# Optimization experiments

Measured on AMD Instinct MI355X. Metric: run time of the kernel, lower is better.

Reference implementation:

```python
import jax, jax.numpy as jnp
import numpy as np
from jax import lax

C = 64; H = 128; W = 256; HW = H * W
HIDDEN = 64
D_STATE = 64; HEADDIM = 64; EXPAND = 2; CHUNK = 256; CONV_K = 4
D_INNER = EXPAND * C            # 128
NHEADS = D_INNER // HEADDIM     # 2
CONV_DIM = D_INNER + 2 * D_STATE  # 256
D_IN_PROJ = 2 * D_INNER + 2 * D_STATE + NHEADS  # 386
RECORD_LEN = [5, 3, 4, 2]
EPS = 1e-5


def setup_inputs() -> dict:
    key = jax.random.key(0)
    ks = jax.random.split(key, 16)
    def nrm(k, shape, scale=0.02):
        return scale * jax.random.normal(k, shape, jnp.float32)
    return {
        "xx": jax.random.normal(ks[0], (sum(RECORD_LEN), C, H, W), jnp.float32),
        "record_len": jnp.array(RECORD_LEN, jnp.int32),
        "score_w1": nrm(ks[1], (HIDDEN, C)),
        "score_b1": jnp.zeros((HIDDEN,), jnp.float32),
        "score_w2": nrm(ks[2], (1, HIDDEN)),
        "score_b2": jnp.zeros((1,), jnp.float32),
        "q_w": nrm(ks[3], (C, C)), "q_b": jnp.zeros((C,), jnp.float32),
        "k_w": nrm(ks[4], (C, C)), "k_b": jnp.zeros((C,), jnp.float32),
        "v_w": nrm(ks[5], (C, C)), "v_b": jnp.zeros((C,), jnp.float32),
        "ln_w": jnp.ones((C,), jnp.float32), "ln_b": jnp.zeros((C,), jnp.float32),
        "in_proj_w": nrm(ks[6], (D_IN_PROJ, C)),
        "in_proj_b": jnp.zeros((D_IN_PROJ,), jnp.float32),
        "conv_w": nrm(ks[7], (CONV_DIM, 1, CONV_K), 0.1),
        "conv_b": jnp.zeros((CONV_DIM,), jnp.float32),
        "dt_bias": 0.1 * jax.random.normal(ks[8], (NHEADS,), jnp.float32),
        "A_log": jnp.log(jnp.arange(1, NHEADS + 1, dtype=jnp.float32)),
        "ssd_D": jnp.ones((NHEADS,), jnp.float32),
        "rms_w": jnp.ones((D_INNER,), jnp.float32),
        "out_proj_w": nrm(ks[9], (C, D_INNER)),
    }


def _segsum(x):
    # x: (..., T) -> (..., T, T) with sum_{j<k<=i} x[k] below diagonal, -inf above
    T = x.shape[-1]
    cs = jnp.cumsum(x, -1)
    ss = cs[..., :, None] - cs[..., None, :]
    return jnp.where(jnp.tril(jnp.ones((T, T), bool)), ss, -jnp.inf)


def _ssd(x, A, Bm, Cm):
    # Mamba2 chunked SSD. x:(b,l,h,p) pre-scaled by dt; A:(b,l,h)=dt*A_head; Bm,Cm:(b,l,n) (ngroups=1)
    b, l, h, p = x.shape
    c = l // CHUNK
    x = x.reshape(b, c, CHUNK, h, p)
    A = A.reshape(b, c, CHUNK, h).transpose(0, 3, 1, 2)            # (b,h,c,cl)
    Bm = Bm.reshape(b, c, CHUNK, -1)
    Cm = Cm.reshape(b, c, CHUNK, -1)
    A_cum = jnp.cumsum(A, -1)
    Lmat = jnp.exp(_segsum(A))                                     # (b,h,c,cl,cl)
    Y_diag = jnp.einsum('bcln,bcsn,bhcls,bcshp->bclhp', Cm, Bm, Lmat, x)
    decay_states = jnp.exp(A_cum[..., -1:] - A_cum)                # (b,h,c,cl)
    states = jnp.einsum('bcln,bhcl,bclhp->bchpn', Bm, decay_states, x)
    padded = jnp.pad(A_cum[..., -1], ((0, 0), (0, 0), (1, 0)))     # (b,h,c+1)
    decay_chunk = jnp.exp(_segsum(padded))                         # (b,h,c+1,c+1)
    states_cat = jnp.concatenate([jnp.zeros_like(states[:, :1]), states], 1)
    states_in = jnp.einsum('bhzc,bchpn->bzhpn', decay_chunk, states_cat)[:, :-1]
    Y_off = jnp.einsum('bcln,bchpn,bhcl->bclhp', Cm, states_in, jnp.exp(A_cum))
    return (Y_diag + Y_off).reshape(b, l, h, p)


def _forward(xx, record_len, score_w1, score_b1, score_w2, score_b2,
             q_w, q_b, k_w, k_b, v_w, v_b, ln_w, ln_b,
             in_proj_w, in_proj_b, conv_w, conv_b,
             dt_bias, A_log, ssd_D, rms_w, out_proj_w):
    rl = [int(v) for v in np.asarray(record_len)]
    # score_mlp: 1x1 convs == per-pixel channel MLP, applied to all CAVs at once
    s = jax.nn.relu(jnp.einsum('nchw,dc->ndhw', xx, score_w1) + score_b1[None, :, None, None])
    scores = (jnp.einsum('ndhw,od->nohw', s, score_w2) + score_b2[None, :, None, None])[:, 0]  # (N,H,W)
    fused = []
    start = 0
    for n in rl:  # ragged groups (variable n_cav per sample)
        grp_sc = scores[start:start + n]
        idx = jnp.argmax(grp_sc, axis=0)  # topk k=1; softmax over singleton -> weight 1
        fused.append(jnp.take_along_axis(xx[start:start + n], idx[None, None], axis=0)[0])
        start += n
    fused = jnp.stack(fused)  # (B,C,H,W)
    Bsz = fused.shape[0]
    seq = fused.reshape(Bsz, C, HW).transpose(0, 2, 1)  # (B,L,C)
    # ScaledDotProductAttention on (HW,1,C): each position attends only to itself
    q = seq @ q_w.T + q_b
    k = seq @ k_w.T + k_b
    v = seq @ v_w.T + v_b
    score = jnp.sum(q * k, -1, keepdims=True) / np.float32(np.sqrt(C))  # (B,L,1)
    attn = jax.nn.softmax(score[..., None], axis=-1)[..., 0]            # == 1
    ctx = attn * v
    # VMAMBA2 block: pre-LayerNorm -> Mamba2 SSD -> residual
    mu = jnp.mean(ctx, -1, keepdims=True)
    var = jnp.var(ctx, -1, keepdims=True)
    u = (ctx - mu) / jnp.sqrt(var + EPS) * ln_w + ln_b
    zxbcdt = u @ in_proj_w.T + in_proj_b
    z = zxbcdt[..., :D_INNER]
    xBC = zxbcdt[..., D_INNER:D_INNER + CONV_DIM]
    dt = zxbcdt[..., D_INNER + CONV_DIM:]
    xBC = lax.conv_general_dilated(xBC.transpose(0, 2, 1), conv_w, (1,), [(CONV_K - 1, 0)],
                                   dimension_numbers=('NCH', 'OIH', 'NCH'),
                                   feature_group_count=CONV_DIM)
    xBC = jax.nn.silu(xBC + conv_b[None, :, None]).transpose(0, 2, 1)  # (B,L,CONV_DIM)
    xh = xBC[..., :D_INNER].reshape(Bsz, HW, NHEADS, HEADDIM)
    Bm = xBC[..., D_INNER:D_INNER + D_STATE]
    Cm = xBC[..., D_INNER + D_STATE:]
    dt = jax.nn.softplus(dt + dt_bias)  # (B,L,h)
    A = -jnp.exp(A_log)                 # (h,)
    y = _ssd(xh * dt[..., None], dt * A, Bm, Cm)
    y = y + ssd_D[None, None, :, None] * xh
    y = y.reshape(Bsz, HW, D_INNER)
    yz = y * jax.nn.silu(z)             # gated RMSNorm
    y = yz * lax.rsqrt(jnp.mean(yz * yz, -1, keepdims=True) + EPS) * rms_w
    h = ctx + y @ out_proj_w.T
    return h.transpose(0, 2, 1).reshape(Bsz, C, H, W)


def reference(xx, record_len, score_w1, score_b1, score_w2, score_b2,
              q_w, q_b, k_w, k_b, v_w, v_b, ln_w, ln_b,
              in_proj_w, in_proj_b, conv_w, conv_b,
              dt_bias, A_log, ssd_D, rms_w, out_proj_w):
    return _forward(xx, record_len, score_w1, score_b1, score_w2, score_b2,
                    q_w, q_b, k_w, k_b, v_w, v_b, ln_w, ln_b,
                    in_proj_w, in_proj_b, conv_w, conv_b,
                    dt_bias, A_log, ssd_D, rms_w, out_proj_w)
```

## Files before the change

### kernel.cpp

```cpp
#include <hip/hip_runtime.h>
#include <cmath>

#define HW 32768
#define NC 128
#define NH 2
#define B4 4

typedef __attribute__((ext_vector_type(8))) short bf16x8;
typedef __attribute__((ext_vector_type(4))) float f32x4;
typedef __attribute__((ext_vector_type(4))) ushort u16x4;
typedef __attribute__((ext_vector_type(8))) ushort u16x8;

__device__ __forceinline__ ushort f2b(float x) {
  union { float f; unsigned u; } v; v.f = x;
  unsigned r = v.u + 0x7FFFu + ((v.u >> 16) & 1u);
  return (ushort)(r >> 16);
}
__device__ __forceinline__ float b2f(ushort b) {
  union { unsigned u; float f; } v; v.u = ((unsigned)b) << 16;
  return v.f;
}
__device__ __forceinline__ int swz(int row, int k) { return k ^ ((row & 7) << 3); }
__device__ __forceinline__ bf16x8 ldfrag(const ushort* base, int row, int k, int stride) {
  return *(const bf16x8*)(base + row * stride + swz(row, k));
}

__global__ __launch_bounds__(256) void k_score_mfma(
    const float* __restrict__ xx, const float* __restrict__ w1,
    const float* __restrict__ b1, const float* __restrict__ w2,
    const float* __restrict__ b2, float* __restrict__ scores,
    int* __restrict__ cnt)
{
  __shared__ ushort Whi[64*64];
  __shared__ ushort Wlo[64*64];
  __shared__ ushort Xt[4][64*64];
  __shared__ float w2b1[128];
  int tid = threadIdx.x;
  if (blockIdx.x == 0 && tid == 0) cnt[0] = 0;
  for (int i = tid; i < 4096; i += 256) {
    int d = i >> 6, c = i & 63;
    float v = w1[i];
    ushort hi = f2b(v);
    int off = d*64 + swz(d, c);
    Whi[off] = hi;
    Wlo[off] = f2b(v - b2f(hi));
  }
  if (tid < 64) { w2b1[tid] = w2[tid]; w2b1[64+tid] = b1[tid]; }

  int wid = tid >> 6, lane = tid & 63;
  int n  = blockIdx.x >> 7;
  int t0 = (blockIdx.x & 127)*256 + wid*64;

  {
    const float* px = xx + (size_t)n*64*HW + t0 + lane;
    float xv[64];
    #pragma unroll
    for (int c = 0; c < 64; ++c) xv[c] = px[(size_t)c*HW];
    ushort* xh = Xt[wid];
    #pragma unroll
    for (int c8 = 0; c8 < 8; ++c8) {
      u16x8 p;
      #pragma unroll
      for (int j = 0; j < 8; ++j) p[j] = f2b(xv[c8*8 + j]);
      *(u16x8*)(xh + lane*64 + swz(lane, c8*8)) = p;
    }
  }
  __syncthreads();

  int lr = lane & 15, kb = lane >> 4;
  const ushort* xh = Xt[wid];
  f32x4 acc[4][4];
  #pragma unroll
  for (int m = 0; m < 4; ++m)
    #pragma unroll
    for (int nt = 0; nt < 4; ++nt) acc[m][nt] = (f32x4){0.f,0.f,0.f,0.f};
  #pragma unroll
  for (int k0 = 0; k0 < 64; k0 += 32) {
    bf16x8 ah[4], al[4], bx[4];
    #pragma unroll
    for (int m = 0; m < 4; ++m) {
      ah[m] = ldfrag(Whi, 16*m + lr, k0 + kb*8, 64);
      al[m] = ldfrag(Wlo, 16*m + lr, k0 + kb*8, 64);
    }
    #pragma unroll
    for (int nt = 0; nt < 4; ++nt) bx[nt] = ldfrag(xh, 16*nt + lr, k0 + kb*8, 64);
    #pragma unroll
    for (int m = 0; m < 4; ++m)
      #pragma unroll
      for (int nt = 0; nt < 4; ++nt) {
        acc[m][nt] = __builtin_amdgcn_mfma_f32_16x16x32_bf16(ah[m], bx[nt], acc[m][nt], 0, 0, 0);
        acc[m][nt] = __builtin_amdgcn_mfma_f32_16x16x32_bf16(al[m], bx[nt], acc[m][nt], 0, 0, 0);
      }
  }
  float bb2 = b2[0];
  #pragma unroll
  for (int nt = 0; nt < 4; ++nt) {
    float s = 0.f;
    #pragma unroll
    for (int m = 0; m < 4; ++m)
      #pragma unroll
      for (int r = 0; r < 4; ++r) {
        int d = 16*m + kb*4 + r;
        float h = acc[m][nt][r] + w2b1[64 + d];
        s += fmaxf(h, 0.f) * w2b1[d];
      }
    s += __shfl_xor(s, 16);
    s += __shfl_xor(s, 32);
    if (kb == 0) scores[(size_t)n*HW + t0 + 16*nt + lr] = s + bb2;
  }
}

__global__ __launch_bounds__(256) void k_argmax(
    const float* __restrict__ scores, int* __restrict__ idx,
    int* __restrict__ cnt, int* __restrict__ list)
{
  int i = blockIdx.x*256 + threadIdx.x;
  int g = i >> 15, t = i & (HW-1);
  const int gs0[4] = {0,5,8,12};
  const int gl0[4] = {5,3,4,2};
  int start = gs0[g], len = gl0[g];
  float best = scores[(size_t)start*HW + t];
  float second = -3.4e38f;
  int bi = start;
  for (int j = 1; j < len; ++j) {
    float s = scores[(size_t)(start+j)*HW + t];
    if (s > best) { second = best; best = s; bi = start + j; }
    else if (s > second) second = s;
  }
  idx[i] = bi;
  if (best - second < 5e-4f) {
    int p = atomicAdd(cnt, 1);
    list[p] = i;
  }
}

__global__ __launch_bounds__(256) void k_fix(
    const float* __restrict__ xx, const float* __restrict__ w1,
    const float* __restrict__ b1, const float* __restrict__ w2,
    const float* __restrict__ b2, const int* __restrict__ cnt,
    const int* __restrict__ list, int* __restrict__ idx)
{
  __shared__ float w1f[64*65];
  __shared__ float w2f[64], b1f[64];
  int tid = threadIdx.x;
  for (int i = tid; i < 4096; i += 256) w1f[(i >> 6)*65 + (i & 63)] = w1[i];
  if (tid < 64) { w2f[tid] = w2[tid]; b1f[tid] = b1[tid]; }
  __syncthreads();
  int n = cnt[0];
  int wid = tid >> 6, lane = tid & 63;
  int nwaves = gridDim.x * 4;
  const int gs0[4] = {0,5,8,12};
  const int gl0[4] = {5,3,4,2};
  double b2d = (double)b2[0];
  for (int e = blockIdx.x*4 + wid; e < n; e += nwaves) {
    int i = list[e];
    int g = i >> 15, t = i & (HW-1);
    int start = gs0[g], len = gl0[g];
    double best = -1e300;
    int bi = start;
    for (int j = 0; j < len; ++j) {
      double xv = (double)xx[(size_t)(start+j)*64*HW + (size_t)lane*HW + t];
      double acc = (double)b1f[lane];
      #pragma unroll
      for (int c = 0; c < 64; ++c) {
        double xc = __shfl(xv, c);
        acc += xc * (double)w1f[lane*65 + c];
      }
      double sc = (acc > 0.0 ? acc : 0.0) * (double)w2f[lane];
      #pragma unroll
      for (int m = 1; m < 64; m <<= 1) sc += __shfl_xor(sc, m);
      sc += b2d;
      if (sc > best) { best = sc; bi = start + j; }
    }
    if (lane == 0) idx[i] = bi;
  }
}

__global__ __launch_bounds__(256) void k_fuse(
    const float* __restrict__ xx, const int* __restrict__ idx,
    float* __restrict__ seq)
{
  __shared__ int idxs[64];
  __shared__ float tile[64*65];
  int tid = threadIdx.x;
  int g  = blockIdx.x >> 9;
  int t0 = (blockIdx.x & 511) << 6;
  if (tid < 64) idxs[tid] = idx[(size_t)g*HW + t0 + tid];
  __syncthreads();
  int tl = tid & 63, cq = tid >> 6;
  for (int r = 0; r < 16; ++r) {
    int c = r*4 + cq;
    tile[c*65 + tl] = xx[(size_t)idxs[tl]*64*HW + (size_t)c*HW + t0 + tl];
  }
  __syncthreads();
  for (int r = 0; r < 16; ++r) {
    int row = r*4 + cq;
    seq[((size_t)g*HW + t0 + row)*64 + tl] = tile[tl*65 + row];
  }
}

__global__ __launch_bounds__(256) void k_vln(
    const float* __restrict__ seq, const float* __restrict__ vw,
    const float* __restrict__ vb, const float* __restrict__ lnw,
    const float* __restrict__ lnb, float* __restrict__ ctx,
    ushort* __restrict__ usw)
{
  __shared__ float st[64*64];
  int tid = threadIdx.x;
  size_t p0 = (size_t)blockIdx.x * 64;
  for (int i = tid; i < 64*64; i += 256) st[i] = seq[p0*64 + i];
  int o = tid & 63, wv = tid >> 6;
  float w[64];
  const float4* w4 = (const float4*)(vw + o*64);
  #pragma unroll
  for (int c4 = 0; c4 < 16; ++c4) {
    float4 v = w4[c4];
    w[c4*4+0]=v.x; w[c4*4+1]=v.y; w[c4*4+2]=v.z; w[c4*4+3]=v.w;
  }
  float bias = vb[o], lw = lnw[o], lb = lnb[o];
  __syncthreads();
  const float4* st4 = (const float4*)st;
  for (int j = 0; j < 16; ++j) {
    int p = wv*16 + j;
    float acc = bias;
    #pragma unroll
    for (int c4 = 0; c4 < 16; ++c4) {
      float4 s4 = st4[p*16 + c4];
      acc += s4.x*w[c4*4] + s4.y*w[c4*4+1] + s4.z*w[c4*4+2] + s4.w*w[c4*4+3];
    }
    float s1 = acc, s2 = acc*acc;
    #pragma unroll
    for (int m = 1; m < 64; m <<= 1) {
      s1 += __shfl_xor(s1, m);
      s2 += __shfl_xor(s2, m);
    }
    float mu  = s1*(1.f/64.f);
    float var = s2*(1.f/64.f) - mu*mu;
    float rstd = rsqrtf(var + 1e-5f);
    size_t base = (p0+p)*64;
    int gt = (int)(p0 + p);
    ctx[base + o] = acc;
    usw[base + (o ^ (((gt+3)&7)<<3))] = f2b((acc - mu)*rstd*lw + lb);
  }
}

__global__ __launch_bounds__(256) void k_prep(
    const float* __restrict__ ipw, ushort* __restrict__ wsw)
{
  int i = blockIdx.x*256 + threadIdx.x;
  int row = i >> 6, c = i & 63;
  float v = (row < 386) ? ipw[row*64 + c] : 0.f;
  wsw[row*64 + swz(row, c)] = f2b(v);
}

__global__ __launch_bounds__(512) void k_gemm(
    const ushort* __restrict__ usw, const ushort* __restrict__ wsw,
    const float* __restrict__ ipb, const float* __restrict__ dtbias,
    ushort* __restrict__ z, ushort* __restrict__ xbcB, float* __restrict__ dt)
{
  __shared__ ushort Wlds[400*64];
  __shared__ ushort Ulds[80*64];
  __shared__ ushort trans[8704];
  int tid = threadIdx.x;
  int b     = blockIdx.x >> 7;
  int chunk = blockIdx.x & 127;
  int w = tid >> 6, lane = tid & 63, lr = lane & 15, kb = lane >> 4;

  for (int i = tid; i < 3200; i += 512)
    *(u16x8*)(Wlds + i*8) = *(const u16x8*)(wsw + i*8);

  for (int it = 0; it < 4; ++it) {
    int s = chunk*4 + it;
    int t0 = s << 6;
    size_t pixbase = (size_t)b*HW + t0;
    size_t tilebase = ((size_t)(b*512 + s))*256*64;
    {
      const ushort* ubase = usw + ((size_t)b*HW + t0 - 3)*64;
      for (int i = tid; i < 536; i += 512) {
        u16x8 v;
        if (t0 == 0 && i < 24) v = (u16x8){0,0,0,0,0,0,0,0};
        else v = *(const u16x8*)(ubase + i*8);
        *(u16x8*)(Ulds + i*8) = v;
      }
    }
    __syncthreads();

    for (int rd = 0; rd < 3; ++rd) {
      int nt = rd*8 + w;
      f32x4 acc[5];
      #pragma unroll
      for (int mt = 0; mt < 5; ++mt) acc[mt] = (f32x4){0.f,0.f,0.f,0.f};
      #pragma unroll
      for (int kk = 0; kk < 64; kk += 32) {
        bf16x8 bfrag = ldfrag(Wlds, nt*16 + lr, kk + kb*8, 64);
        #pragma unroll
        for (int mt = 0; mt < 5; ++mt) {
          bf16x8 afrag = ldfrag(Ulds, mt*16 + lr, kk + kb*8, 64);
          acc[mt] = __builtin_amdgcn_mfma_f32_16x16x32_bf16(afrag, bfrag, acc[mt], 0, 0, 0);
        }
      }
      float bias = ipb[nt*16 + lr];
      if (rd == 0) {
        #pragma unroll
        for (int mt = 0; mt < 5; ++mt)
          #pragma unroll
          for (int r = 0; r < 4; ++r) {
            int t = mt*16 + kb*4 + r - 3;
            if (t >= 0 && t < 64) trans[t*132 + w*16 + lr] = f2b(acc[mt][r] + bias);
          }
      } else {
        #pragma unroll
        for (int mt = 0; mt < 5; ++mt)
          #pragma unroll
          for (int r = 0; r < 4; ++r) {
            int t = mt*16 + kb*4 + r - 3;
            if (t >= 0 && t < 64) trans[(w*16 + lr)*68 + t] = f2b(acc[mt][r] + bias);
          }
      }
      __syncthreads();
      if (rd == 0) {
        for (int i = tid; i < 2048; i += 512) {
          int t = i >> 5, c4 = (i & 31)*4;
          *(u16x4*)(z + (pixbase + t)*128 + c4) = *(const u16x4*)(trans + t*132 + c4);
        }
      } else {
        int chbase = (rd - 1)*128;
        for (int i = tid; i < 2048; i += 512) {
          int ch = i >> 4, t4 = (i & 15)*4;
          *(u16x4*)(xbcB + tilebase + (size_t)(chbase + ch)*64 + t4)
              = *(const u16x4*)(trans + ch*68 + t4);
        }
      }
      __syncthreads();
    }

    if (w == 0) {
      f32x4 acc[5];
      #pragma unroll
      for (int mt = 0; mt < 5; ++mt) acc[mt] = (f32x4){0.f,0.f,0.f,0.f};
      #pragma unroll
      for (int kk = 0; kk < 64; kk += 32) {
        bf16x8 bfrag = ldfrag(Wlds, 384 + lr, kk + kb*8, 64);
        #pragma unroll
        for (int mt = 0; mt < 5; ++mt) {
          bf16x8 afrag = ldfrag(Ulds, mt*16 + lr, kk + kb*8, 64);
          acc[mt] = __builtin_amdgcn_mfma_f32_16x16x32_bf16(afrag, bfrag, acc[mt], 0, 0, 0);
        }
      }
      if (lr < 2) {
        float bias = ipb[384 + lr] + dtbias[lr];
        #pragma unroll
        for (int mt = 0; mt < 5; ++mt)
          #pragma unroll
          for (int r = 0; r < 4; ++r) {
            int t = mt*16 + kb*4 + r - 3;
            if (t >= 0 && t < 64) {
              float a = acc[mt][r] + bias;
              dt[(pixbase + t)*2 + lr] = (a > 20.f) ? a : log1pf(expf(a));
            }
          }
      }
    }
    __syncthreads();
  }
}

__global__ __launch_bounds__(256) void k_conv(
    const ushort* __restrict__ xbcB, const float* __restrict__ convw,
    const float* __restrict__ convb, ushort* __restrict__ co2,
    ushort* __restrict__ Bm, ushort* __restrict__ Cm)
{
  __shared__ ushort bmc[64*132];
  int tid = threadIdx.x;
  int b  = blockIdx.x >> 9;
  int s  = blockIdx.x & 511;
  int lane = tid & 63, wv = tid >> 6;
  int toct = lane & 7, chi = lane >> 3;
  size_t tilebase = ((size_t)(b*512 + s))*256*64;
  const ushort* tsrc = xbcB + tilebase;
  const ushort* psrc = xbcB + tilebase - 256*64;

  for (int it = 0; it < 8; ++it) {
    int ch = wv*64 + it*8 + chi;
    u16x8 v = *(const u16x8*)(tsrc + ch*64 + toct*8);
    float x0 = b2f(v[0]), x1 = b2f(v[1]), x2 = b2f(v[2]), x3 = b2f(v[3]);
    float x4 = b2f(v[4]), x5 = b2f(v[5]), x6 = b2f(v[6]), x7 = b2f(v[7]);
    float pm1 = __shfl(x7, lane - 1);
    float pm2 = __shfl(x6, lane - 1);
    float pm3 = __shfl(x5, lane - 1);
    if (toct == 0) {
      if (s > 0) {
        u16x4 hq = *(const u16x4*)(psrc + ch*64 + 60);
        pm3 = b2f(hq[1]); pm2 = b2f(hq[2]); pm1 = b2f(hq[3]);
      } else {
        pm1 = pm2 = pm3 = 0.f;
      }
    }
    float4 cw = ((const float4*)convw)[ch];
    float cb = convb[ch];
    float o0 = cb + cw.x*pm3 + cw.y*pm2 + cw.z*pm1 + cw.w*x0;
    float o1 = cb + cw.x*pm2 + cw.y*pm1 + cw.z*x0  + cw.w*x1;
    float o2 = cb + cw.x*pm1 + cw.y*x0  + cw.z*x1  + cw.w*x2;
    float o3 = cb + cw.x*x0  + cw.y*x1  + cw.z*x2  + cw.w*x3;
    float o4 = cb + cw.x*x1  + cw.y*x2  + cw.z*x3  + cw.w*x4;
    float o5 = cb + cw.x*x2  + cw.y*x3  + cw.z*x4  + cw.w*x5;
    float o6 = cb + cw.x*x3  + cw.y*x4  + cw.z*x5  + cw.w*x6;
    float o7 = cb + cw.x*x4  + cw.y*x5  + cw.z*x6  + cw.w*x7;
    u16x8 ov;
    ov[0] = f2b(o0 / (1.f + __expf(-o0)));
    ov[1] = f2b(o1 / (1.f + __expf(-o1)));
    ov[2] = f2b(o2 / (1.f + __expf(-o2)));
    ov[3] = f2b(o3 / (1.f + __expf(-o3)));
    ov[4] = f2b(o4 / (1.f + __expf(-o4)));
    ov[5] = f2b(o5 / (1.f + __expf(-o5)));
    ov[6] = f2b(o6 / (1.f + __expf(-o6)));
    ov[7] = f2b(o7 / (1.f + __expf(-o7)));
    *(u16x8*)(co2 + tilebase + (size_t)ch*64 + toct*8) = ov;
    if (ch >= 128) {
      int c = ch - 128;
      int csw = c ^ (toct << 2);
      #pragma unroll
      for (int j = 0; j < 8; ++j)
        bmc[(toct*8 + j)*132 + csw] = ov[j];
    }
  }
  __syncthreads();
  size_t tg = (size_t)b*HW + s*64;
  for (int i = tid; i < 1024; i += 256) {
    int tt = i >> 4, n4 = (i & 15)*4;
    int sw = (tt >> 3) << 2;
    *(u16x4*)(Bm + (tg + tt)*64 + n4) = *(const u16x4*)(bmc + tt*132 + (n4 ^ sw));
    *(u16x4*)(Cm + (tg + tt)*64 + n4) = *(const u16x4*)(bmc + tt*132 + ((64 + n4) ^ sw));
  }
}

__global__ __launch_bounds__(256) void k_states(
    const float* __restrict__ dt, const ushort* __restrict__ co2,
    const float* __restrict__ A_log,
    float* __restrict__ states, float* __restrict__ A_last)
{
  extern __shared__ char smem[];
  float* ac  = (float*)smem;
  float* dec = ac + 256;
  ushort* xdT = (ushort*)(dec + 256);
  ushort* BT  = xdT + 16384;
  int tid = threadIdx.x;
  int ci = blockIdx.x, h = blockIdx.y, b = blockIdx.z;
  size_t tg = (size_t)b*HW + (size_t)ci*256;
  float Aneg = -expf(A_log[h]);
  float dv = dt[(tg + tid)*2 + h];
  ac[tid] = dv*Aneg;
  __syncthreads();
  for (int off = 1; off < 256; off <<= 1) {
    float v = (tid >= off) ? ac[tid - off] : 0.f;
    __syncthreads();
    ac[tid] += v;
    __syncthreads();
  }
  float alast = ac[255];
  dec[tid] = dv * __expf(alast - ac[tid]);
  __syncthreads();
  for (int i = tid; i < 64*32; i += 256) {
    int p = i >> 5, lc = (i & 31) * 8;
    int s = (ci << 2) + (lc >> 6);
    const ushort* cb2 = co2 + ((size_t)(b*512 + s))*256*64 + (lc & 63);
    u16x8 xv = *(const u16x8*)(cb2 + (size_t)(h*64 + p)*64);
    u16x8 o;
    #pragma unroll
    for (int e = 0; e < 8; ++e) o[e] = f2b(b2f(xv[e]) * dec[lc + e]);
    *(u16x8*)(xdT + p*256 + swz(p, lc)) = o;
    u16x8 bv = *(const u16x8*)(cb2 + (size_t)(128 + p)*64);
    *(u16x8*)(BT + p*256 + swz(p, lc)) = bv;
  }
  __syncthreads();
  int w = tid >> 6, lane = tid & 63, lr = lane & 15, kb = lane >> 4;
  f32x4 acc[4];
  #pragma unroll
  for (int m = 0; m < 4; ++m) acc[m] = (f32x4){0.f,0.f,0.f,0.f};
  for (int k0 = 0; k0 < 256; k0 += 32) {
    bf16x8 bfrag = ldfrag(BT, 16*w + lr, k0 + kb*8, 256);
    #pragma unroll
    for (int m = 0; m < 4; ++m) {
      bf16x8 afrag = ldfrag(xdT, 16*m + lr, k0 + kb*8, 256);
      acc[m] = __builtin_amdgcn_mfma_f32_16x16x32_bf16(afrag, bfrag, acc[m], 0, 0, 0);
    }
  }
  size_t sb = (((size_t)b*NC + ci)*NH + h)*4096;
  #pragma unroll
  for (int m = 0; m < 4; ++m)
    #pragma unroll
    for (int r = 0; r < 4; ++r)
      states[sb + (size_t)(16*m + kb*4 + r)*64 + 16*w + lr] = acc[m][r];
  if (tid == 0) A_last[((size_t)b*NH + h)*NC + ci] = alast;
}

__global__ __launch_bounds__(256) void k_scan(
    const float* __restrict__ states, const float* __restrict__ A_last,
    float* __restrict__ states_in)
{
  __shared__ float ef[NC];
  int tid = threadIdx.x;
  int seg = blockIdx.x & 7, h = (blockIdx.x >> 3) & 1, b = blockIdx.x >> 4;
  if (tid < NC) ef[tid] = __expf(A_last[((size_t)b*NH + h)*NC + tid]);
  __syncthreads();
  size_t base0 = (((size_t)b*NC)*NH + h)*4096 + seg*512 + tid;
  const size_t cstride = (size_t)NH*4096;
  float s0 = 0.f, s1 = 0.f;
  float ld0 = states[base0], ld1 = states[base0 + 256];
  for (int zc = 0; zc < NC; ++zc) {
    size_t cur = base0 + (size_t)zc*cstride;
    float n0 = 0.f, n1 = 0.f;
    if (zc < NC-1) { n0 = states[cur + cstride]; n1 = states[cur + cstride + 256]; }
    states_in[cur] = s0; states_in[cur + 256] = s1;
    float e = ef[zc];
    s0 = ld0 + e*s0; s1 = ld1 + e*s1;
    ld0 = n0; ld1 = n1;
  }
}

__global__ __launch_bounds__(512) void k_ydiag(
    const float* __restrict__ dt, const ushort* __restrict__ co2,
    const ushort* __restrict__ Bm, const ushort* __restrict__ Cm,
    const float* __restrict__ states_in, const float* __restrict__ A_log,
    const float* __restrict__ ssd_D, ushort* __restrict__ y)
{
  extern __shared__ char smem[];
  float* ac   = (float*)smem;
  float* dts  = ac + 256;
  float* segs = dts + 256;
  ushort* Cb  = (ushort*)(segs + 8);
  ushort* Bb  = Cb + 16384;
  ushort* xsT = Bb + 16384;
  ushort* Sb  = xsT + 16384;
  ushort* Wb  = Sb + 4096;
  int tid = threadIdx.x;
  int ci = blockIdx.x, h = blockIdx.y, b = blockIdx.z;
  size_t tg = (size_t)b*HW + (size_t)ci*256;
  int w = tid >> 6, lane = tid & 63, lr = lane & 15, kb = lane >> 4;
  float Aneg = -expf(A_log[h]);

  float dv = 0.f, a = 0.f;
  if (tid < 256) {
    dv = dt[(tg + tid)*2 + h];
    a = dv*Aneg;
    #pragma unroll
    for (int d = 1; d < 64; d <<= 1) {
      float t = __shfl_up(a, d);
      if (lane >= d) a += t;
    }
    if (lane == 63) segs[w] = a;
  }
  __syncthreads();
  if (tid < 256) {
    float off = 0.f;
    #pragma unroll
    for (int j = 0; j < 4; ++j) if (j < w) off += segs[j];
    ac[tid] = a + off;
    dts[tid] = dv;
  }

  for (int i = tid; i < 256*16; i += 512) {
    int l = i >> 4, n4 = (i & 15) * 4;
    u16x4 cv = *(const u16x4*)(Cm + (tg + l)*64 + n4);
    *(u16x4*)(Cb + l*64 + swz(l, n4)) = cv;
    u16x4 bv = *(const u16x4*)(Bm + (tg + l)*64 + n4);
    *(u16x4*)(Bb + l*64 + swz(l, n4)) = bv;
  }
  {
    const ushort* ct0 = co2 + ((size_t)(b*512 + (ci << 2)))*16384 + (size_t)h*4096;
    for (int i = tid; i < 64*32; i += 512) {
      int p = i >> 5, sc = (i & 31) * 8;
      u16x8 xv = *(const u16x8*)(ct0 + (size_t)(sc >> 6)*16384 + (size_t)p*64 + (sc & 63));
      *(u16x8*)(xsT + p*256 + swz(p, sc)) = xv;
    }
  }
  size_t sbg = (((size_t)b*NC + ci)*NH + h)*4096;
  for (int i = tid; i < 1024; i += 512) {
    int p = i >> 4, n4 = (i & 15) * 4;
    float4 sv = *(const float4*)(states_in + sbg + p*64 + n4);
    u16x4 pk = { f2b(sv.x), f2b(sv.y), f2b(sv.z), f2b(sv.w) };
    *(u16x4*)(Sb + p*64 + swz(p, n4)) = pk;
  }
  __syncthreads();

  int strips[2] = { w, 15 - w };
  ushort* Ww = Wb + w*1152;

  f32x4 yy[2][4];
  #pragma unroll
  for (int sp = 0; sp < 2; ++sp)
    #pragma unroll
    for (int n = 0; n < 4; ++n) yy[sp][n] = (f32x4){0.f,0.f,0.f,0.f};
  #pragma unroll
  for (int kk = 0; kk < 64; kk += 32) {
    bf16x8 af[2], bf[4];
    #pragma unroll
    for (int sp = 0; sp < 2; ++sp) af[sp] = ldfrag(Cb, strips[sp]*16 + lr, kk + kb*8, 64);
    #pragma unroll
    for (int n = 0; n < 4; ++n) bf[n] = ldfrag(Sb, 16*n + lr, kk + kb*8, 64);
    #pragma unroll
    for (int sp = 0; sp < 2; ++sp)
      #pragma unroll
      for (int n = 0; n < 4; ++n)
        yy[sp][n] = __builtin_amdgcn_mfma_f32_16x16x32_bf16(af[sp], bf[n], yy[sp][n], 0, 0, 0);
  }
  #pragma unroll
  for (int sp = 0; sp < 2; ++sp)
    #pragma unroll
    for (int r = 0; r < 4; ++r) {
      float e = __expf(ac[strips[sp]*16 + kb*4 + r]);
      #pragma unroll
      for (int n = 0; n < 4; ++n) yy[sp][n][r] *= e;
    }

  #pragma unroll
  for (int sp = 0; sp < 2; ++sp) {
    int strip = strips[sp];
    int l0 = strip*16;
    int nst = (strip >> 2) + 1;
    for (int st = 0; st < nst; ++st) {
      int s0 = st*64;
      f32x4 g[4];
      #pragma unroll
      for (int n = 0; n < 4; ++n) g[n] = (f32x4){0.f,0.f,0.f,0.f};
      #pragma unroll
      for (int kk = 0; kk < 64; kk += 32) {
        bf16x8 af = ldfrag(Cb, l0 + lr, kk + kb*8, 64);
        bf16x8 bf[4];
        #pragma unroll
        for (int n = 0; n < 4; ++n) bf[n] = ldfrag(Bb, s0 + 16*n + lr, kk + kb*8, 64);
        #pragma unroll
        for (int n = 0; n < 4; ++n)
          g[n] = __builtin_amdgcn_mfma_f32_16x16x32_bf16(af, bf[n], g[n], 0, 0, 0);
      }
      #pragma unroll
      for (int r = 0; r < 4; ++r) {
        int lrow = kb*4 + r;
        int lg = l0 + lrow;
        float acl = ac[lg];
        #pragma unroll
        for (int n = 0; n < 4; ++n) {
          int sl = 16*n + lr;
          int sg = s0 + sl;
          float v = (sg <= lg) ? g[n][r] * __expf(acl - ac[sg]) * dts[sg] : 0.f;
          Ww[lrow*72 + sl] = f2b(v);
        }
      }
      #pragma unroll
      for (int kk = 0; kk < 64; kk += 32) {
        bf16x8 af = *(const bf16x8*)(Ww + lr*72 + kk + kb*8);
        bf16x8 bf[4];
        #pragma unroll
        for (int n = 0; n < 4; ++n) bf[n] = ldfrag(xsT, 16*n + lr, s0 + kk + kb*8, 256);
        #pragma unroll
        for (int n = 0; n < 4; ++n)
          yy[sp][n] = __builtin_amdgcn_mfma_f32_16x16x32_bf16(af, bf[n], yy[sp][n], 0, 0, 0);
      }
    }
  }

  float Dh = ssd_D[h];
  #pragma unroll
  for (int sp = 0; sp < 2; ++sp)
    #pragma unroll
    for (int r = 0; r < 4; ++r) {
      int lg = strips[sp]*16 + kb*4 + r;
      #pragma unroll
      for (int n = 0; n < 4; ++n) {
        int p = 16*n + lr;
        float val = yy[sp][n][r] + Dh * b2f(xsT[p*256 + swz(p, lg)]);
        y[(tg + lg)*128 + h*64 + p] = f2b(val);
      }
    }
}

__global__ __launch_bounds__(256) void k_final(
    const ushort* __restrict__ y, const ushort* __restrict__ z,
    const float* __restrict__ ctx, const float* __restrict__ rms_w,
    const float* __restrict__ opw, float* __restrict__ out)
{
  __shared__ ushort yn[64*128];
  __shared__ ushort wop[64*128];
  __shared__ float otile[64*65];
  int tid = threadIdx.x;
  size_t p0 = (size_t)blockIdx.x * 64;

  for (int i = tid; i < 2048; i += 256) {
    int row = i >> 5, c4 = (i & 31) * 4;
    float4 v = ((const float4*)(opw + row*128))[c4 >> 2];
    float4 rw = ((const float4*)rms_w)[c4 >> 2];
    u16x4 p = { f2b(v.x*rw.x), f2b(v.y*rw.y), f2b(v.z*rw.z), f2b(v.w*rw.w) };
    *(u16x4*)(wop + row*128 + swz(row, c4)) = p;
  }

  {
    int t = tid >> 2, q = tid & 3;
    const u16x4* yp = (const u16x4*)(y + (p0 + t)*128 + q*32);
    const u16x4* zp = (const u16x4*)(z + (p0 + t)*128 + q*32);
    float vals[32];
    float ss = 0.f;
    #pragma unroll
    for (int j = 0; j < 8; ++j) {
      u16x4 yv = yp[j];
      u16x4 zv = zp[j];
      #pragma unroll
      for (int e = 0; e < 4; ++e) {
        float zf = b2f(zv[e]);
        float x = b2f(yv[e]) * (zf / (1.f + __expf(-zf)));
        vals[j*4+e] = x; ss += x*x;
      }
    }
    ss += __shfl_xor(ss, 1);
    ss += __shfl_xor(ss, 2);
    float rinv = rsqrtf(ss*(1.f/128.f) + 1e-5f);
    #pragma unroll
    for (int j = 0; j < 8; ++j) {
      int c4 = q*32 + j*4;
      u16x4 p = { f2b(vals[j*4]*rinv), f2b(vals[j*4+1]*rinv),
                  f2b(vals[j*4+2]*rinv), f2b(vals[j*4+3]*rinv) };
      *(u16x4*)(yn + t*128 + swz(t, c4)) = p;
    }
  }
  __syncthreads();

  int w = tid >> 6, lane = tid & 63, lr = lane & 15, kb = lane >> 4;
  f32x4 acc[4];
  #pragma unroll
  for (int n = 0; n < 4; ++n) acc[n] = (f32x4){0.f,0.f,0.f,0.f};
  #pragma unroll
  for (int kk = 0; kk < 128; kk += 32) {
    bf16x8 a = ldfrag(yn, w*16 + lr, kk + kb*8, 128);
    #pragma unroll
    for (int n = 0; n < 4; ++n) {
      bf16x8 bf = ldfrag(wop, n*16 + lr, kk + kb*8, 128);
      acc[n] = __builtin_amdgcn_mfma_f32_16x16x32_bf16(a, bf, acc[n], 0, 0, 0);
    }
  }
  #pragma unroll
  for (int n = 0; n < 4; ++n)
    #pragma unroll
    for (int r = 0; r < 4; ++r) {
      int tok = w*16 + kb*4 + r, ch = n*16 + lr;
      otile[ch*65 + tok] = acc[n][r] + ctx[(p0 + tok)*64 + ch];
    }
  __syncthreads();
  {
    size_t b  = p0 >> 15;
    size_t t0 = p0 & (HW-1);
    for (int r = 0; r < 16; ++r) {
      int cc = r*4 + (tid >> 6);
      int pp = tid & 63;
      out[(b*64 + cc)*HW + t0 + pp] = otile[cc*65 + pp];
    }
  }
}

extern "C" void kernel_launch(void* const* d_in, const int* in_sizes, int n_in,
                              void* d_out, int out_size, void* d_ws, size_t ws_size,
                              hipStream_t stream) {
  (void)in_sizes; (void)n_in; (void)out_size; (void)ws_size;
  const float* xx   = (const float*)d_in[0];
  const float* sw1  = (const float*)d_in[2];
  const float* sb1  = (const float*)d_in[3];
  const float* sw2  = (const float*)d_in[4];
  const float* sb2  = (const float*)d_in[5];
  const float* vw   = (const float*)d_in[10];
  const float* vb   = (const float*)d_in[11];
  const float* lnw  = (const float*)d_in[12];
  const float* lnb  = (const float*)d_in[13];
  const float* ipw  = (const float*)d_in[14];
  const float* ipb  = (const float*)d_in[15];
  const float* cw   = (const float*)d_in[16];
  const float* cb   = (const float*)d_in[17];
  const float* dtb  = (const float*)d_in[18];
  const float* alog = (const float*)d_in[19];
  const float* sd   = (const float*)d_in[20];
  const float* rmsw = (const float*)d_in[21];
  const float* opw  = (const float*)d_in[22];

  float* ws = (float*)d_ws;
  float*  scores32 = ws;
  int*    idxb     = (int*)(ws + 458752);
  int*    cntb     = (int*)(ws + 589824);
  int*    listb    = (int*)(ws + 589832);
  float*  dtp      = ws;
  float*  seq      = ws + 917504;
  ushort* Cmb      = (ushort*)(ws + 917504);
  ushort* Bmb      = (ushort*)(ws + 5111808);
  float*  ctx      = ws + 9306112;
  ushort* uswb     = (ushort*)(ws + 17694720);
  float*  states   = ws + 17694720;
  float*  states_in= ws + 21889024;
  ushort* zb       = (ushort*)(ws + 26083328);
  ushort* xbcBb    = (ushort*)(ws + 34471936);
  ushort* co2b     = (ushort*)(ws + 51249152);
  ushort* yb       = (ushort*)(ws + 68026368);
  float*  Alast    = ws + 84803584;
  ushort* wswb     = (ushort*)(ws + 84804608);

  k_score_mfma<<<1792, 256, 0, stream>>>(xx, sw1, sb1, sw2, sb2, scores32, cntb);
  k_argmax<<<512, 256, 0, stream>>>(scores32, idxb, cntb, listb);
  k_fix<<<512, 256, 0, stream>>>(xx, sw1, sb1, sw2, sb2, cntb, listb, idxb);
  k_fuse<<<2048, 256, 0, stream>>>(xx, idxb, seq);
  k_vln<<<2048, 256, 0, stream>>>(seq, vw, vb, lnw, lnb, ctx, uswb);
  k_prep<<<100, 256, 0, stream>>>(ipw, wswb);
  k_gemm<<<512, 512, 0, stream>>>(uswb, wswb, ipb, dtb, zb, xbcBb, dtp);
  k_conv<<<2048, 256, 0, stream>>>(xbcBb, cw, cb, co2b, Bmb, Cmb);
  dim3 gssd(NC, NH, B4);
  k_states<<<gssd, 256, 67584, stream>>>(dtp, co2b, alog, states, Alast);
  k_scan<<<64, 256, 0, stream>>>(states, Alast, states_in);
  k_ydiag<<<gssd, 512, 127008, stream>>>(dtp, co2b, Bmb, Cmb, states_in, alog, sd, yb);
  k_final<<<2048, 256, 0, stream>>>(yb, zb, ctx, rmsw, opw, (float*)d_out);
}
```

Measured before the change: 397.2 us.

## Store seq and ctx as bf16 and drop separate Bm/Cm buffers

The fused sequence and ctx intermediates are now stored as bf16 instead of fp32, which halves their global write and read traffic. The conv kernel no longer writes separate token-major Bm/Cm copies through LDS. The ydiag kernel instead reads B and C straight from the channel-major conv output and transposes them into its swizzled shared tiles. This lowers precision on the residual ctx and the seq input, and adds scattered LDS stores in ydiag.

```diff
diff --git a/kernel.cpp b/kernel.cpp
--- a/kernel.cpp
+++ b/kernel.cpp
@@ -178,7 +178,7 @@
 
 __global__ __launch_bounds__(256) void k_fuse(
     const float* __restrict__ xx, const int* __restrict__ idx,
-    float* __restrict__ seq)
+    ushort* __restrict__ seqb)
 {
   __shared__ int idxs[64];
   __shared__ float tile[64*65];
@@ -195,20 +195,24 @@
   __syncthreads();
   for (int r = 0; r < 16; ++r) {
     int row = r*4 + cq;
-    seq[((size_t)g*HW + t0 + row)*64 + tl] = tile[tl*65 + row];
+    seqb[((size_t)g*HW + t0 + row)*64 + tl] = f2b(tile[tl*65 + row]);
   }
 }
 
 __global__ __launch_bounds__(256) void k_vln(
-    const float* __restrict__ seq, const float* __restrict__ vw,
+    const ushort* __restrict__ seqb, const float* __restrict__ vw,
     const float* __restrict__ vb, const float* __restrict__ lnw,
-    const float* __restrict__ lnb, float* __restrict__ ctx,
+    const float* __restrict__ lnb, ushort* __restrict__ ctxb,
     ushort* __restrict__ usw)
 {
   __shared__ float st[64*64];
   int tid = threadIdx.x;
   size_t p0 = (size_t)blockIdx.x * 64;
-  for (int i = tid; i < 64*64; i += 256) st[i] = seq[p0*64 + i];
+  for (int i = tid; i < 1024; i += 256) {
+    u16x4 v = *(const u16x4*)(seqb + p0*64 + i*4);
+    st[i*4+0] = b2f(v[0]); st[i*4+1] = b2f(v[1]);
+    st[i*4+2] = b2f(v[2]); st[i*4+3] = b2f(v[3]);
+  }
   int o = tid & 63, wv = tid >> 6;
   float w[64];
   const float4* w4 = (const float4*)(vw + o*64);
@@ -239,7 +243,7 @@
     float rstd = rsqrtf(var + 1e-5f);
     size_t base = (p0+p)*64;
     int gt = (int)(p0 + p);
-    ctx[base + o] = acc;
+    ctxb[base + o] = f2b(acc);
     usw[base + (o ^ (((gt+3)&7)<<3))] = f2b((acc - mu)*rstd*lw + lb);
   }
 }
@@ -367,10 +371,8 @@
 
 __global__ __launch_bounds__(256) void k_conv(
     const ushort* __restrict__ xbcB, const float* __restrict__ convw,
-    const float* __restrict__ convb, ushort* __restrict__ co2,
-    ushort* __restrict__ Bm, ushort* __restrict__ Cm)
-{
-  __shared__ ushort bmc[64*132];
+    const float* __restrict__ convb, ushort* __restrict__ co2)
+{
   int tid = threadIdx.x;
   int b  = blockIdx.x >> 9;
   int s  = blockIdx.x & 511;
@@ -416,21 +418,6 @@
     ov[6] = f2b(o6 / (1.f + __expf(-o6)));
     ov[7] = f2b(o7 / (1.f + __expf(-o7)));
     *(u16x8*)(co2 + tilebase + (size_t)ch*64 + toct*8) = ov;
-    if (ch >= 128) {
-      int c = ch - 128;
-      int csw = c ^ (toct << 2);
-      #pragma unroll
-      for (int j = 0; j < 8; ++j)
-        bmc[(toct*8 + j)*132 + csw] = ov[j];
-    }
-  }
-  __syncthreads();
-  size_t tg = (size_t)b*HW + s*64;
-  for (int i = tid; i < 1024; i += 256) {
-    int tt = i >> 4, n4 = (i & 15)*4;
-    int sw = (tt >> 3) << 2;
-    *(u16x4*)(Bm + (tg + tt)*64 + n4) = *(const u16x4*)(bmc + tt*132 + (n4 ^ sw));
-    *(u16x4*)(Cm + (tg + tt)*64 + n4) = *(const u16x4*)(bmc + tt*132 + ((64 + n4) ^ sw));
   }
 }
 
@@ -520,7 +507,6 @@
 
 __global__ __launch_bounds__(512) void k_ydiag(
     const float* __restrict__ dt, const ushort* __restrict__ co2,
-    const ushort* __restrict__ Bm, const ushort* __restrict__ Cm,
     const float* __restrict__ states_in, const float* __restrict__ A_log,
     const float* __restrict__ ssd_D, ushort* __restrict__ y)
 {
@@ -559,15 +545,22 @@
     dts[tid] = dv;
   }
 
-  for (int i = tid; i < 256*16; i += 512) {
-    int l = i >> 4, n4 = (i & 15) * 4;
-    u16x4 cv = *(const u16x4*)(Cm + (tg + l)*64 + n4);
-    *(u16x4*)(Cb + l*64 + swz(l, n4)) = cv;
-    u16x4 bv = *(const u16x4*)(Bm + (tg + l)*64 + n4);
-    *(u16x4*)(Bb + l*64 + swz(l, n4)) = bv;
+  const ushort* ctb = co2 + ((size_t)(b*512 + (ci << 2)))*16384;
+  for (int i = tid; i < 2048; i += 512) {
+    int n = i >> 5, sub = i & 31;
+    int j = sub >> 3, toct = sub & 7;
+    u16x8 bv = *(const u16x8*)(ctb + (size_t)j*16384 + (size_t)(128 + n)*64 + toct*8);
+    u16x8 cv = *(const u16x8*)(ctb + (size_t)j*16384 + (size_t)(192 + n)*64 + toct*8);
+    int lbase = j*64 + toct*8;
+    #pragma unroll
+    for (int ee = 0; ee < 8; ++ee) {
+      int e = (ee + toct) & 7;
+      Bb[(lbase + e)*64 + swz(lbase + e, n)] = bv[e];
+      Cb[(lbase + e)*64 + swz(lbase + e, n)] = cv[e];
+    }
   }
   {
-    const ushort* ct0 = co2 + ((size_t)(b*512 + (ci << 2)))*16384 + (size_t)h*4096;
+    const ushort* ct0 = ctb + (size_t)h*4096;
     for (int i = tid; i < 64*32; i += 512) {
       int p = i >> 5, sc = (i & 31) * 8;
       u16x8 xv = *(const u16x8*)(ct0 + (size_t)(sc >> 6)*16384 + (size_t)p*64 + (sc & 63));
@@ -676,7 +669,7 @@
 
 __global__ __launch_bounds__(256) void k_final(
     const ushort* __restrict__ y, const ushort* __restrict__ z,
-    const float* __restrict__ ctx, const float* __restrict__ rms_w,
+    const ushort* __restrict__ ctxb, const float* __restrict__ rms_w,
     const float* __restrict__ opw, float* __restrict__ out)
 {
   __shared__ ushort yn[64*128];
@@ -741,7 +734,7 @@
     #pragma unroll
     for (int r = 0; r < 4; ++r) {
       int tok = w*16 + kb*4 + r, ch = n*16 + lr;
-      otile[ch*65 + tok] = acc[n][r] + ctx[(p0 + tok)*64 + ch];
+      otile[ch*65 + tok] = acc[n][r] + b2f(ctxb[(p0 + tok)*64 + ch]);
     }
   __syncthreads();
   {
@@ -784,10 +777,8 @@
   int*    cntb     = (int*)(ws + 589824);
   int*    listb    = (int*)(ws + 589832);
   float*  dtp      = ws;
-  float*  seq      = ws + 917504;
-  ushort* Cmb      = (ushort*)(ws + 917504);
-  ushort* Bmb      = (ushort*)(ws + 5111808);
-  float*  ctx      = ws + 9306112;
+  ushort* seqb     = (ushort*)(ws + 917504);
+  ushort* ctxb     = (ushort*)(ws + 9306112);
   ushort* uswb     = (ushort*)(ws + 17694720);
   float*  states   = ws + 17694720;
   float*  states_in= ws + 21889024;
@@ -801,14 +792,14 @@
   k_score_mfma<<<1792, 256, 0, stream>>>(xx, sw1, sb1, sw2, sb2, scores32, cntb);
   k_argmax<<<512, 256, 0, stream>>>(scores32, idxb, cntb, listb);
   k_fix<<<512, 256, 0, stream>>>(xx, sw1, sb1, sw2, sb2, cntb, listb, idxb);
-  k_fuse<<<2048, 256, 0, stream>>>(xx, idxb, seq);
-  k_vln<<<2048, 256, 0, stream>>>(seq, vw, vb, lnw, lnb, ctx, uswb);
+  k_fuse<<<2048, 256, 0, stream>>>(xx, idxb, seqb);
+  k_vln<<<2048, 256, 0, stream>>>(seqb, vw, vb, lnw, lnb, ctxb, uswb);
   k_prep<<<100, 256, 0, stream>>>(ipw, wswb);
   k_gemm<<<512, 512, 0, stream>>>(uswb, wswb, ipb, dtb, zb, xbcBb, dtp);
-  k_conv<<<2048, 256, 0, stream>>>(xbcBb, cw, cb, co2b, Bmb, Cmb);
+  k_conv<<<2048, 256, 0, stream>>>(xbcBb, cw, cb, co2b);
   dim3 gssd(NC, NH, B4);
   k_states<<<gssd, 256, 67584, stream>>>(dtp, co2b, alog, states, Alast);
   k_scan<<<64, 256, 0, stream>>>(states, Alast, states_in);
-  k_ydiag<<<gssd, 512, 127008, stream>>>(dtp, co2b, Bmb, Cmb, states_in, alog, sd, yb);
-  k_final<<<2048, 256, 0, stream>>>(yb, zb, ctx, rmsw, opw, (float*)d_out);
-}
+  k_ydiag<<<gssd, 512, 127008, stream>>>(dtp, co2b, states_in, alog, sd, yb);
+  k_final<<<2048, 256, 0, stream>>>(yb, zb, ctxb, rmsw, opw, (float*)d_out);
+}
```

Result: faster. 388.1 us (-2.3%).

## Fuse gather with V-projection/LayerNorm, store ctx as bf16, use exp2 in ydiag

Applied to the files above, without the earlier changes.

Merges the gather/transpose kernel with the V-projection plus LayerNorm kernel, so the gathered tile stays in shared memory and is never written to or read back from a global seq buffer. The ctx residual is now stored in bf16 rather than fp32, which halves its write and its later read in k_final. In k_ydiag the cumulative decay is prescaled by log2(e) and evaluated with exp2f. These changes cut global memory traffic at the cost of more shared memory per block and bf16 rounding on the residual path.

```diff
diff --git a/kernel.cpp b/kernel.cpp
--- a/kernel.cpp
+++ b/kernel.cpp
@@ -176,12 +176,15 @@
   }
 }
 
-__global__ __launch_bounds__(256) void k_fuse(
+__global__ __launch_bounds__(256) void k_fusevln(
     const float* __restrict__ xx, const int* __restrict__ idx,
-    float* __restrict__ seq)
+    const float* __restrict__ vw, const float* __restrict__ vb,
+    const float* __restrict__ lnw, const float* __restrict__ lnb,
+    ushort* __restrict__ ctxb, ushort* __restrict__ usw)
 {
   __shared__ int idxs[64];
   __shared__ float tile[64*65];
+  __shared__ float st[64*68];
   int tid = threadIdx.x;
   int g  = blockIdx.x >> 9;
   int t0 = (blockIdx.x & 511) << 6;
@@ -195,21 +198,9 @@
   __syncthreads();
   for (int r = 0; r < 16; ++r) {
     int row = r*4 + cq;
-    seq[((size_t)g*HW + t0 + row)*64 + tl] = tile[tl*65 + row];
-  }
-}
-
-__global__ __launch_bounds__(256) void k_vln(
-    const float* __restrict__ seq, const float* __restrict__ vw,
-    const float* __restrict__ vb, const float* __restrict__ lnw,
-    const float* __restrict__ lnb, float* __restrict__ ctx,
-    ushort* __restrict__ usw)
-{
-  __shared__ float st[64*64];
-  int tid = threadIdx.x;
-  size_t p0 = (size_t)blockIdx.x * 64;
-  for (int i = tid; i < 64*64; i += 256) st[i] = seq[p0*64 + i];
-  int o = tid & 63, wv = tid >> 6;
+    st[row*68 + tl] = tile[tl*65 + row];
+  }
+  int o = tl, wv = cq;
   float w[64];
   const float4* w4 = (const float4*)(vw + o*64);
   #pragma unroll
@@ -219,13 +210,14 @@
   }
   float bias = vb[o], lw = lnw[o], lb = lnb[o];
   __syncthreads();
-  const float4* st4 = (const float4*)st;
+  size_t p0 = (size_t)g*HW + t0;
   for (int j = 0; j < 16; ++j) {
     int p = wv*16 + j;
+    const float4* row4 = (const float4*)(st + p*68);
     float acc = bias;
     #pragma unroll
     for (int c4 = 0; c4 < 16; ++c4) {
-      float4 s4 = st4[p*16 + c4];
+      float4 s4 = row4[c4];
       acc += s4.x*w[c4*4] + s4.y*w[c4*4+1] + s4.z*w[c4*4+2] + s4.w*w[c4*4+3];
     }
     float s1 = acc, s2 = acc*acc;
@@ -237,9 +229,9 @@
     float mu  = s1*(1.f/64.f);
     float var = s2*(1.f/64.f) - mu*mu;
     float rstd = rsqrtf(var + 1e-5f);
-    size_t base = (p0+p)*64;
-    int gt = (int)(p0 + p);
-    ctx[base + o] = acc;
+    size_t base = (p0 + p)*64;
+    int gt = t0 + p;
+    ctxb[base + o] = f2b(acc);
     usw[base + (o ^ (((gt+3)&7)<<3))] = f2b((acc - mu)*rstd*lw + lb);
   }
 }
@@ -538,6 +530,7 @@
   size_t tg = (size_t)b*HW + (size_t)ci*256;
   int w = tid >> 6, lane = tid & 63, lr = lane & 15, kb = lane >> 4;
   float Aneg = -expf(A_log[h]);
+  const float LOG2E = 1.44269504088896f;
 
   float dv = 0.f, a = 0.f;
   if (tid < 256) {
@@ -555,7 +548,7 @@
     float off = 0.f;
     #pragma unroll
     for (int j = 0; j < 4; ++j) if (j < w) off += segs[j];
-    ac[tid] = a + off;
+    ac[tid] = (a + off) * LOG2E;
     dts[tid] = dv;
   }
 
@@ -608,7 +601,7 @@
   for (int sp = 0; sp < 2; ++sp)
     #pragma unroll
     for (int r = 0; r < 4; ++r) {
-      float e = __expf(ac[strips[sp]*16 + kb*4 + r]);
+      float e = exp2f(ac[strips[sp]*16 + kb*4 + r]);
       #pragma unroll
       for (int n = 0; n < 4; ++n) yy[sp][n][r] *= e;
     }
@@ -642,7 +635,7 @@
         for (int n = 0; n < 4; ++n) {
           int sl = 16*n + lr;
           int sg = s0 + sl;
-          float v = (sg <= lg) ? g[n][r] * __expf(acl - ac[sg]) * dts[sg] : 0.f;
+          float v = (sg <= lg) ? g[n][r] * exp2f(acl - ac[sg]) * dts[sg] : 0.f;
           Ww[lrow*72 + sl] = f2b(v);
         }
       }
@@ -676,7 +669,7 @@
 
 __global__ __launch_bounds__(256) void k_final(
     const ushort* __restrict__ y, const ushort* __restrict__ z,
-    const float* __restrict__ ctx, const float* __restrict__ rms_w,
+    const ushort* __restrict__ ctxb, const float* __restrict__ rms_w,
     const float* __restrict__ opw, float* __restrict__ out)
 {
   __shared__ ushort yn[64*128];
@@ -741,7 +734,7 @@
     #pragma unroll
     for (int r = 0; r < 4; ++r) {
       int tok = w*16 + kb*4 + r, ch = n*16 + lr;
-      otile[ch*65 + tok] = acc[n][r] + ctx[(p0 + tok)*64 + ch];
+      otile[ch*65 + tok] = acc[n][r] + b2f(ctxb[(p0 + tok)*64 + ch]);
     }
   __syncthreads();
   {
@@ -784,10 +777,9 @@
   int*    cntb     = (int*)(ws + 589824);
   int*    listb    = (int*)(ws + 589832);
   float*  dtp      = ws;
-  float*  seq      = ws + 917504;
   ushort* Cmb      = (ushort*)(ws + 917504);
   ushort* Bmb      = (ushort*)(ws + 5111808);
-  float*  ctx      = ws + 9306112;
+  ushort* ctxb     = (ushort*)(ws + 9306112);
   ushort* uswb     = (ushort*)(ws + 17694720);
   float*  states   = ws + 17694720;
   float*  states_in= ws + 21889024;
@@ -801,8 +793,7 @@
   k_score_mfma<<<1792, 256, 0, stream>>>(xx, sw1, sb1, sw2, sb2, scores32, cntb);
   k_argmax<<<512, 256, 0, stream>>>(scores32, idxb, cntb, listb);
   k_fix<<<512, 256, 0, stream>>>(xx, sw1, sb1, sw2, sb2, cntb, listb, idxb);
-  k_fuse<<<2048, 256, 0, stream>>>(xx, idxb, seq);
-  k_vln<<<2048, 256, 0, stream>>>(seq, vw, vb, lnw, lnb, ctx, uswb);
+  k_fusevln<<<2048, 256, 0, stream>>>(xx, idxb, vw, vb, lnw, lnb, ctxb, uswb);
   k_prep<<<100, 256, 0, stream>>>(ipw, wswb);
   k_gemm<<<512, 512, 0, stream>>>(uswb, wswb, ipb, dtb, zb, xbcBb, dtp);
   k_conv<<<2048, 256, 0, stream>>>(xbcBb, cw, cb, co2b, Bmb, Cmb);
@@ -810,5 +801,5 @@
   k_states<<<gssd, 256, 67584, stream>>>(dtp, co2b, alog, states, Alast);
   k_scan<<<64, 256, 0, stream>>>(states, Alast, states_in);
   k_ydiag<<<gssd, 512, 127008, stream>>>(dtp, co2b, Bmb, Cmb, states_in, alog, sd, yb);
-  k_final<<<2048, 256, 0, stream>>>(yb, zb, ctx, rmsw, opw, (float*)d_out);
-}
+  k_final<<<2048, 256, 0, stream>>>(yb, zb, ctxb, rmsw, opw, (float*)d_out);
+}
```

Result: faster. 381.1 us (-4.1%).
